# Kernel tuning notes

Hardware: AMD Instinct MI355X
Metric: run time of the kernel (lower is better)

## Reference

```python
import jax, jax.numpy as jnp
import numpy as np

N, E, IN_DIM, H, D = 50000, 1600000, 128, 8, 16


def setup_inputs() -> dict:
    key = jax.random.key(0)
    ks = jax.random.split(key, 9)
    s = 1.0 / np.sqrt(IN_DIM)
    return {
        "h": jax.random.normal(ks[0], (N, IN_DIM), dtype=jnp.float32),
        "Wq": jax.random.normal(ks[1], (IN_DIM, H * D), dtype=jnp.float32) * s,
        "bq": jax.random.normal(ks[2], (H * D,), dtype=jnp.float32) * 0.01,
        "Wk": jax.random.normal(ks[3], (IN_DIM, H * D), dtype=jnp.float32) * s,
        "bk": jax.random.normal(ks[4], (H * D,), dtype=jnp.float32) * 0.01,
        "Wv": jax.random.normal(ks[5], (IN_DIM, H * D), dtype=jnp.float32) * s,
        "bv": jax.random.normal(ks[6], (H * D,), dtype=jnp.float32) * 0.01,
        "src": jax.random.randint(ks[7], (E,), 0, N, dtype=jnp.int32),
        "dst": jax.random.randint(ks[8], (E,), 0, N, dtype=jnp.int32),
    }


def reference(h, Wq, bq, Wk, bk, Wv, bv, src, dst):
    n = h.shape[0]
    # node-level projections, reshaped to [N, H, D]
    Q = (h @ Wq + bq).reshape(n, H, D)
    K = (h @ Wk + bk).reshape(n, H, D)
    V = (h @ Wv + bv).reshape(n, H, D)
    # per-edge score: dot(K[src], Q[dst]) / sqrt(D), exp-clamped -> [E, H]
    score = jnp.sum(K[src] * Q[dst], axis=-1) / np.sqrt(D)
    score = jnp.exp(jnp.clip(score, -5.0, 5.0))
    # score-weighted messages scattered into destination nodes
    m = V[src] * score[:, :, None]                    # [E, H, D]
    wV = jax.ops.segment_sum(m, dst, num_segments=n)  # [N, H, D]
    z = jax.ops.segment_sum(score, dst, num_segments=n)  # [N, H]
    h_out = wV / (z[:, :, None] + 1e-6)
    return h_out.reshape(n, H * D)
```

## Files before the change

### kernel.cpp

```cpp
#include <hip/hip_runtime.h>
#include <hip/hip_bf16.h>

#define IN_DIM 128
#define HH 8
#define DD 16
#define HD 128
#define SCAN_B 256
#define CHUNK 8192

#define MT  64
#define KP  128

typedef float f32x4 __attribute__((ext_vector_type(4)));
typedef short s16x8 __attribute__((ext_vector_type(8)));

__device__ __forceinline__ int sniff_fp32(const unsigned short* h_raw) {
  int sane = 0;
#pragma unroll
  for (int i = 0; i < 128; i += 2) {
    const unsigned short u = h_raw[i];
    const int expo = (u >> 7) & 0xFF;
    if (expo >= 112 && expo <= 143) sane++;
  }
  return (sane >= 40) ? 0 : 1;
}

__global__ __launch_bounds__(128) void wt_kernel(
    const unsigned short* __restrict__ h_raw,
    const void* __restrict__ Wq, const void* __restrict__ Wk,
    const void* __restrict__ Wv, __hip_bfloat16* __restrict__ Wt,
    int* __restrict__ flag, int* __restrict__ bucket_size) {
  const int isf = sniff_fp32(h_raw);
  const int n = blockIdx.x;
  const int k = threadIdx.x;
  if (n == 0) {
    if (k == 0) *flag = isf;
    for (int j = k; j < 258; j += 128) bucket_size[j] = 0;
  }
  const int mat = n >> 7;
  const int col = n & 127;
  const void* W = (mat == 0) ? Wq : (mat == 1) ? Wk : Wv;
  float v;
  if (isf) v = ((const float*)W)[(size_t)k * HD + col];
  else     v = __bfloat162float(((const __hip_bfloat16*)W)[(size_t)k * HD + col]);
  Wt[(size_t)n * KP + k] = __float2bfloat16(v);
}

__global__ __launch_bounds__(256) void proj_hist_kernel(
    const void* __restrict__ h, const __hip_bfloat16* __restrict__ Wt,
    const void* __restrict__ bq, const void* __restrict__ bk,
    const void* __restrict__ bv,
    __hip_bfloat16* __restrict__ Qb, __hip_bfloat16* __restrict__ Kb,
    __hip_bfloat16* __restrict__ Vb,
    const int* __restrict__ flag, int n_nodes,
    const int* __restrict__ dst, int* __restrict__ bucket_size, int n_edges,
    int pgrid) {
  __shared__ int lh[256];

  const int tid = threadIdx.x;

  if (blockIdx.x >= pgrid) {
    const int e0 = (blockIdx.x - pgrid) * CHUNK;
    const int e1 = (e0 + CHUNK < n_edges) ? e0 + CHUNK : n_edges;
    lh[tid] = 0;
    __syncthreads();
    for (int e = e0 + tid; e < e1; e += 256) atomicAdd(&lh[dst[e] >> 8], 1);
    __syncthreads();
    if (lh[tid] > 0) atomicAdd(&bucket_size[tid], lh[tid]);
    return;
  }

  const int node0 = blockIdx.x * MT;
  const int isf = *flag;

  const int wave = tid >> 6;
  const int lane = tid & 63;
  const int l15 = lane & 15;
  const int quad = lane >> 4;

  const int g = node0 + wave * 16 + l15;
  const int gs = (g < n_nodes) ? g : (n_nodes - 1);
  s16x8 afrag[4];
  if (isf) {
    const float* hp = (const float*)h + (size_t)gs * HD;
#pragma unroll
    for (int k4 = 0; k4 < 4; ++k4) {
      const f32x4 a0 = *(const f32x4*)(hp + k4 * 32 + quad * 8);
      const f32x4 a1 = *(const f32x4*)(hp + k4 * 32 + quad * 8 + 4);
      s16x8 fr;
#pragma unroll
      for (int j = 0; j < 4; ++j) {
        const __hip_bfloat16 b0 = __float2bfloat16(a0[j]);
        const __hip_bfloat16 b1 = __float2bfloat16(a1[j]);
        fr[j] = *(const short*)&b0;
        fr[4 + j] = *(const short*)&b1;
      }
      afrag[k4] = fr;
    }
  } else {
    const __hip_bfloat16* hp = (const __hip_bfloat16*)h + (size_t)gs * HD;
#pragma unroll
    for (int k4 = 0; k4 < 4; ++k4)
      afrag[k4] = *(const s16x8*)(hp + k4 * 32 + quad * 8);
  }

  for (int c = 0; c < 3; ++c) {
    const __hip_bfloat16* wb = Wt + (size_t)c * 128 * KP;

    f32x4 acc[8];
#pragma unroll
    for (int t = 0; t < 8; ++t) acc[t] = (f32x4){0.f, 0.f, 0.f, 0.f};

#pragma unroll
    for (int t = 0; t < 8; ++t) {
#pragma unroll
      for (int k4 = 0; k4 < 4; ++k4) {
        const s16x8 bfrag =
            *(const s16x8*)(wb + (t * 16 + l15) * KP + k4 * 32 + quad * 8);
        acc[t] = __builtin_amdgcn_mfma_f32_16x16x32_bf16(afrag[k4], bfrag,
                                                         acc[t], 0, 0, 0);
      }
    }

    const void* bp = (c == 0) ? bq : (c == 1) ? bk : bv;
    __hip_bfloat16* outp = (c == 0) ? Qb : (c == 1) ? Kb : Vb;
#pragma unroll
    for (int t = 0; t < 8; ++t) {
      const int ncol = t * 16 + l15;
      const float bias = isf ? ((const float*)bp)[ncol]
                             : __bfloat162float(((const __hip_bfloat16*)bp)[ncol]);
#pragma unroll
      for (int r = 0; r < 4; ++r) {
        const int gw = node0 + wave * 16 + quad * 4 + r;
        if (gw < n_nodes)
          outp[(size_t)gw * HD + ncol] = __float2bfloat16(acc[t][r] + bias);
      }
    }
  }
}

__global__ __launch_bounds__(256) void bucket_scan_kernel(
    const int* __restrict__ bucket_size, int* __restrict__ bucket_base,
    int* __restrict__ bucket_cur, int nbuck, int n_edges) {
  __shared__ int sh[256];
  const int t = threadIdx.x;
  const int v = (t < nbuck) ? bucket_size[t] : 0;
  sh[t] = v;
  __syncthreads();
  for (int off = 1; off < 256; off <<= 1) {
    int add = (t >= off) ? sh[t - off] : 0;
    __syncthreads();
    sh[t] += add;
    __syncthreads();
  }
  const int excl = sh[t] - v;
  if (t < nbuck) {
    bucket_base[t] = excl;
    bucket_cur[t] = excl;
  }
  if (t == 0) bucket_base[nbuck] = n_edges;
}

__global__ __launch_bounds__(256) void bucketize_kernel(
    const int* __restrict__ src, const int* __restrict__ dst,
    int* __restrict__ bucket_cur, unsigned int* __restrict__ ebuf,
    int n_edges) {
  __shared__ int lh[256];
  const int t = threadIdx.x;
  const int e0 = blockIdx.x * CHUNK;
  const int e1 = (e0 + CHUNK < n_edges) ? e0 + CHUNK : n_edges;
  lh[t] = 0;
  __syncthreads();
  for (int e = e0 + t; e < e1; e += 256) atomicAdd(&lh[dst[e] >> 8], 1);
  __syncthreads();
  const int cnt_local = lh[t];
  int base = 0;
  if (cnt_local > 0) base = atomicAdd(&bucket_cur[t], cnt_local);
  __syncthreads();
  lh[t] = base;
  __syncthreads();
  for (int e = e0 + t; e < e1; e += 256) {
    const int d = dst[e];
    const int pos = atomicAdd(&lh[d >> 8], 1);
    ebuf[pos] = ((unsigned int)src[e] << 16) | (unsigned int)d;
  }
}

__global__ __launch_bounds__(256) void bucket_csr_kernel(
    const unsigned int* __restrict__ ebuf, const int* __restrict__ bucket_base,
    int* __restrict__ row_ptr, int* __restrict__ edge_src,
    int n_nodes, int nbuck) {
  __shared__ int lc[256];
  __shared__ int sh[256];
  const int b = blockIdx.x;
  const int t = threadIdx.x;
  const int lo = bucket_base[b], hi = bucket_base[b + 1];
  const int nbase = b << 8;

  lc[t] = 0;
  __syncthreads();
  for (int i = lo + t; i < hi; i += 256)
    atomicAdd(&lc[(ebuf[i] & 0xFFFFu) - nbase], 1);
  __syncthreads();

  const int v = lc[t];
  sh[t] = v;
  __syncthreads();
  for (int off = 1; off < 256; off <<= 1) {
    int add = (t >= off) ? sh[t - off] : 0;
    __syncthreads();
    sh[t] += add;
    __syncthreads();
  }
  const int excl = sh[t] - v;

  const int node = nbase + t;
  if (node < n_nodes) row_ptr[node] = lo + excl;
  if (b == nbuck - 1 && t == 255) row_ptr[n_nodes] = hi;

  __syncthreads();
  lc[t] = lo + excl;
  __syncthreads();
  for (int i = lo + t; i < hi; i += 256) {
    const unsigned int pkd = ebuf[i];
    const int pos = atomicAdd(&lc[(pkd & 0xFFFFu) - nbase], 1);
    edge_src[pos] = (int)(pkd >> 16);
  }
}

__global__ __launch_bounds__(256) void hist_kernel(
    const int* __restrict__ dst, int* __restrict__ cnt, int n_edges) {
  const int e = blockIdx.x * blockDim.x + threadIdx.x;
  if (e < n_edges) atomicAdd(&cnt[dst[e]], 1);
}

__global__ __launch_bounds__(256) void scatter_kernel(
    const int* __restrict__ src, const int* __restrict__ dst,
    int* __restrict__ cursor, int* __restrict__ edge_src, int n_edges) {
  const int e = blockIdx.x * blockDim.x + threadIdx.x;
  if (e < n_edges) {
    const int pos = atomicAdd(&cursor[dst[e]], 1);
    edge_src[pos] = src[e];
  }
}

__global__ __launch_bounds__(SCAN_B) void scan1_kernel(
    const int* __restrict__ cnt, int* __restrict__ exs,
    int* __restrict__ bsum, int n) {
  __shared__ int sh[SCAN_B];
  const int t = threadIdx.x;
  const int i = blockIdx.x * SCAN_B + t;
  int v = (i < n) ? cnt[i] : 0;
  sh[t] = v;
  __syncthreads();
  for (int off = 1; off < SCAN_B; off <<= 1) {
    int add = (t >= off) ? sh[t - off] : 0;
    __syncthreads();
    sh[t] += add;
    __syncthreads();
  }
  if (i < n) exs[i] = sh[t] - v;
  if (t == SCAN_B - 1) bsum[blockIdx.x] = sh[t];
}

__global__ __launch_bounds__(SCAN_B) void scan2_kernel(int* __restrict__ bsum,
                                                       int nb) {
  __shared__ int sh[SCAN_B];
  const int t = threadIdx.x;
  if (nb <= SCAN_B) {
    int v = (t < nb) ? bsum[t] : 0;
    sh[t] = v;
    __syncthreads();
    for (int off = 1; off < SCAN_B; off <<= 1) {
      int add = (t >= off) ? sh[t - off] : 0;
      __syncthreads();
      sh[t] += add;
      __syncthreads();
    }
    if (t < nb) bsum[t] = sh[t] - v;
  } else if (t == 0) {
    int run = 0;
    for (int b = 0; b < nb; ++b) { int v = bsum[b]; bsum[b] = run; run += v; }
  }
}

__global__ __launch_bounds__(SCAN_B) void scan3_kernel(
    const int* __restrict__ exs, const int* __restrict__ bsum,
    int* __restrict__ row_ptr, int* __restrict__ cursor, int n, int n_edges) {
  const int i = blockIdx.x * SCAN_B + threadIdx.x;
  if (i < n) {
    const int v = exs[i] + bsum[blockIdx.x];
    row_ptr[i] = v;
    cursor[i] = v;
  }
  if (i == 0) row_ptr[n] = n_edges;
}

__global__ __launch_bounds__(128) void gather_kernel(
    const int* __restrict__ row_ptr, const int* __restrict__ edge_src,
    const __hip_bfloat16* __restrict__ Qb, const __hip_bfloat16* __restrict__ Kb,
    const __hip_bfloat16* __restrict__ Vb,
    void* __restrict__ out, const int* __restrict__ flag, int n_nodes) {
  __shared__ float2 sc[2][16 * HH];
  __shared__ float zred[16 * HH];

  const int d = blockIdx.x;
  const int tid = threadIdx.x;

  const int eloc = tid >> 3;
  const int hh8  = tid & 7;
  const int hd16 = tid >> 4;

  const int start = row_ptr[d];
  const int deg = row_ptr[d + 1] - start;

  float qreg[16];
  {
    const uint4* qp = (const uint4*)(Qb + (size_t)d * HD + hh8 * 16);
    unsigned int qw[8];
    *(uint4*)&qw[0] = qp[0];
    *(uint4*)&qw[4] = qp[1];
#pragma unroll
    for (int i = 0; i < 8; ++i) {
      qreg[2 * i]     = __uint_as_float(qw[i] << 16) * 0.25f;
      qreg[2 * i + 1] = __uint_as_float(qw[i] & 0xFFFF0000u) * 0.25f;
    }
  }

  float accV = 0.0f;
  float zacc = 0.0f;
  const int ngroups = (deg + 15) >> 4;

  for (int g = 0; g < ngroups; ++g) {
    const int buf = g & 1;
    const int ei = g * 16 + eloc;

    float score = 0.0f;
    int s = 0;
    if (ei < deg) {
      s = edge_src[start + ei];
      const uint4* kp = (const uint4*)(Kb + (size_t)s * HD + hh8 * 16);
      unsigned int kw[8];
      *(uint4*)&kw[0] = kp[0];
      *(uint4*)&kw[4] = kp[1];
      float dot = 0.0f;
#pragma unroll
      for (int i = 0; i < 8; ++i) {
        const float klo = __uint_as_float(kw[i] << 16);
        const float khi = __uint_as_float(kw[i] & 0xFFFF0000u);
        dot = fmaf(qreg[2 * i], klo, dot);
        dot = fmaf(qreg[2 * i + 1], khi, dot);
      }
      score = __expf(fminf(fmaxf(dot, -5.0f), 5.0f));
    }
    zacc += score;
    sc[buf][eloc * HH + hh8] = make_float2(score, __int_as_float(s));
    __syncthreads();

    const int rem = deg - g * 16;
    const int lim = (rem < 16) ? rem : 16;
    if (lim == 16) {
#pragma unroll
      for (int e = 0; e < 16; ++e) {
        const float2 pe = sc[buf][e * HH + hd16];
        const int s2 = __float_as_int(pe.y);
        const unsigned short vu =
            *(const unsigned short*)(Vb + (size_t)s2 * HD + tid);
        accV = fmaf(pe.x, __uint_as_float(((unsigned int)vu) << 16), accV);
      }
    } else {
      for (int e = 0; e < lim; ++e) {
        const float2 pe = sc[buf][e * HH + hd16];
        const int s2 = __float_as_int(pe.y);
        const unsigned short vu =
            *(const unsigned short*)(Vb + (size_t)s2 * HD + tid);
        accV = fmaf(pe.x, __uint_as_float(((unsigned int)vu) << 16), accV);
      }
    }
  }

  zred[eloc * HH + hh8] = zacc;
  __syncthreads();
  float aZ = 0.0f;
#pragma unroll
  for (int i = 0; i < 16; ++i) aZ += zred[i * HH + hd16];

  const float r = accV / (aZ + 1e-6f);
  const size_t o = (size_t)d * HD + tid;
  if (*flag) ((float*)out)[o] = r;
  else       ((__hip_bfloat16*)out)[o] = __float2bfloat16(r);
}

extern "C" void kernel_launch(void* const* d_in, const int* in_sizes, int n_in,
                              void* d_out, int out_size, void* d_ws, size_t ws_size,
                              hipStream_t stream) {
  const void* h  = d_in[0];
  const void* Wq = d_in[1];
  const void* bq = d_in[2];
  const void* Wk = d_in[3];
  const void* bk = d_in[4];
  const void* Wv = d_in[5];
  const void* bv = d_in[6];
  const int* src = (const int*)d_in[7];
  const int* dst = (const int*)d_in[8];

  const int n_nodes = in_sizes[0] / IN_DIM;
  const int n_edges = in_sizes[7];
  const int nb = (n_nodes + SCAN_B - 1) / SCAN_B;
  const int nbuck = (n_nodes + 255) >> 8;

  char* p = (char*)d_ws;
  int* flag = (int*)p;                       p += 256;
  __hip_bfloat16* Qb = (__hip_bfloat16*)p;   p += (size_t)n_nodes * HD * 2;
  __hip_bfloat16* Kb = (__hip_bfloat16*)p;   p += (size_t)n_nodes * HD * 2;
  __hip_bfloat16* Vb = (__hip_bfloat16*)p;   p += (size_t)n_nodes * HD * 2;
  __hip_bfloat16* Wt = (__hip_bfloat16*)p;   p += ((size_t)384 * KP * 2 + 255) / 256 * 256;
  int* bucket_size = (int*)p;                p += 258 * 4;
  int* bucket_base = (int*)p;                p += 258 * 4;
  int* bucket_cur = (int*)p;                 p += 258 * 4;
  int* row_ptr = (int*)p;                    p += (size_t)(n_nodes + 1) * 4;
  unsigned int* ebuf = (unsigned int*)p;     p += (size_t)n_edges * 4;
  int* edge_src = (int*)p;                   p += (size_t)n_edges * 4;
  int* cnt = (int*)p;                        p += (size_t)n_nodes * 4;
  int* exs = (int*)p;                        p += (size_t)n_nodes * 4;
  int* bsum = (int*)p;                       p += (size_t)(nb + 1) * 4;
  int* cursor = (int*)p;                     p += (size_t)n_nodes * 4;

  wt_kernel<<<384, 128, 0, stream>>>((const unsigned short*)h, Wq, Wk, Wv, Wt,
                                     flag, bucket_size);

  const int pgrid = (n_nodes + MT - 1) / MT;
  const int nchunk = (n_edges + CHUNK - 1) / CHUNK;

  if (n_nodes <= 65536) {
    proj_hist_kernel<<<pgrid + nchunk, 256, 0, stream>>>(
        h, Wt, bq, bk, bv, Qb, Kb, Vb, flag, n_nodes, dst, bucket_size,
        n_edges, pgrid);
    bucket_scan_kernel<<<1, 256, 0, stream>>>(bucket_size, bucket_base,
                                              bucket_cur, nbuck, n_edges);
    bucketize_kernel<<<nchunk, 256, 0, stream>>>(src, dst, bucket_cur, ebuf,
                                                 n_edges);
    bucket_csr_kernel<<<nbuck, 256, 0, stream>>>(ebuf, bucket_base, row_ptr,
                                                 edge_src, n_nodes, nbuck);
  } else {
    proj_hist_kernel<<<pgrid, 256, 0, stream>>>(
        h, Wt, bq, bk, bv, Qb, Kb, Vb, flag, n_nodes, dst, bucket_size,
        n_edges, pgrid);
    hipMemsetAsync(cnt, 0, (size_t)n_nodes * sizeof(int), stream);
    const int eb = 256;
    const int egrid = (n_edges + eb - 1) / eb;
    hist_kernel<<<egrid, eb, 0, stream>>>(dst, cnt, n_edges);
    scan1_kernel<<<nb, SCAN_B, 0, stream>>>(cnt, exs, bsum, n_nodes);
    scan2_kernel<<<1, SCAN_B, 0, stream>>>(bsum, nb);
    scan3_kernel<<<nb, SCAN_B, 0, stream>>>(exs, bsum, row_ptr, cursor,
                                            n_nodes, n_edges);
    scatter_kernel<<<egrid, eb, 0, stream>>>(src, dst, cursor, edge_src,
                                             n_edges);
  }

  gather_kernel<<<n_nodes, 128, 0, stream>>>(row_ptr, edge_src, Qb, Kb, Vb,
                                             d_out, flag, n_nodes);
}
```

Before: 325.1 us.

## Fuse bucket scan into histogram, register-cache bucketize, pack two nodes per gather block

The bucket prefix scan is folded into the histogram blocks of the projection kernel: the last chunk to finish, detected with an atomic counter, performs the scan, which removes one kernel launch. Bucketize now uses smaller chunks and keeps the packed src/dst words in registers, so the second pass no longer rereads src and dst from global memory. The gather kernel processes two destination nodes per 256-thread block and prefetches the next edge_src index a group ahead. Both halves of a block loop to the larger of the two degrees, so some work is wasted on imbalanced node pairs, and the last-block scan depends on correct fence and atomic ordering.

```diff
diff --git a/kernel.cpp b/kernel.cpp
--- a/kernel.cpp
+++ b/kernel.cpp
@@ -7,6 +7,7 @@
 #define HD 128
 #define SCAN_B 256
 #define CHUNK 8192
+#define CHUNK2 2048
 
 #define MT  64
 #define KP  128
@@ -53,24 +54,50 @@
     __hip_bfloat16* __restrict__ Qb, __hip_bfloat16* __restrict__ Kb,
     __hip_bfloat16* __restrict__ Vb,
     const int* __restrict__ flag, int n_nodes,
-    const int* __restrict__ dst, int* __restrict__ bucket_size, int n_edges,
-    int pgrid) {
+    const int* __restrict__ dst, int* __restrict__ bucket_size,
+    int* __restrict__ bucket_base, int* __restrict__ bucket_cur,
+    int n_edges, int nchunk, int nbuck) {
   __shared__ int lh[256];
+  __shared__ int sh[256];
+  __shared__ int is_last;
 
   const int tid = threadIdx.x;
 
-  if (blockIdx.x >= pgrid) {
-    const int e0 = (blockIdx.x - pgrid) * CHUNK;
+  if (blockIdx.x < nchunk) {
+    const int e0 = blockIdx.x * CHUNK;
     const int e1 = (e0 + CHUNK < n_edges) ? e0 + CHUNK : n_edges;
     lh[tid] = 0;
     __syncthreads();
     for (int e = e0 + tid; e < e1; e += 256) atomicAdd(&lh[dst[e] >> 8], 1);
     __syncthreads();
     if (lh[tid] > 0) atomicAdd(&bucket_size[tid], lh[tid]);
+    __threadfence();
+    if (tid == 0) {
+      const int old = atomicAdd(&bucket_size[256], 1);
+      is_last = (old == nchunk - 1);
+    }
+    __syncthreads();
+    if (!is_last) return;
+
+    const int v = (tid < nbuck) ? atomicAdd(&bucket_size[tid], 0) : 0;
+    sh[tid] = v;
+    __syncthreads();
+    for (int off = 1; off < 256; off <<= 1) {
+      int add = (tid >= off) ? sh[tid - off] : 0;
+      __syncthreads();
+      sh[tid] += add;
+      __syncthreads();
+    }
+    const int excl = sh[tid] - v;
+    if (tid < nbuck) {
+      bucket_base[tid] = excl;
+      bucket_cur[tid] = excl;
+    }
+    if (tid == 0) bucket_base[nbuck] = n_edges;
     return;
   }
 
-  const int node0 = blockIdx.x * MT;
+  const int node0 = (blockIdx.x - nchunk) * MT;
   const int isf = *flag;
 
   const int wave = tid >> 6;
@@ -137,28 +164,6 @@
       }
     }
   }
-}
-
-__global__ __launch_bounds__(256) void bucket_scan_kernel(
-    const int* __restrict__ bucket_size, int* __restrict__ bucket_base,
-    int* __restrict__ bucket_cur, int nbuck, int n_edges) {
-  __shared__ int sh[256];
-  const int t = threadIdx.x;
-  const int v = (t < nbuck) ? bucket_size[t] : 0;
-  sh[t] = v;
-  __syncthreads();
-  for (int off = 1; off < 256; off <<= 1) {
-    int add = (t >= off) ? sh[t - off] : 0;
-    __syncthreads();
-    sh[t] += add;
-    __syncthreads();
-  }
-  const int excl = sh[t] - v;
-  if (t < nbuck) {
-    bucket_base[t] = excl;
-    bucket_cur[t] = excl;
-  }
-  if (t == 0) bucket_base[nbuck] = n_edges;
 }
 
 __global__ __launch_bounds__(256) void bucketize_kernel(
@@ -167,11 +172,20 @@
     int n_edges) {
   __shared__ int lh[256];
   const int t = threadIdx.x;
-  const int e0 = blockIdx.x * CHUNK;
-  const int e1 = (e0 + CHUNK < n_edges) ? e0 + CHUNK : n_edges;
+  const int e0 = blockIdx.x * CHUNK2;
+  const int e1 = (e0 + CHUNK2 < n_edges) ? e0 + CHUNK2 : n_edges;
   lh[t] = 0;
   __syncthreads();
-  for (int e = e0 + t; e < e1; e += 256) atomicAdd(&lh[dst[e] >> 8], 1);
+  unsigned int pk[CHUNK2 / 256];
+#pragma unroll
+  for (int j = 0; j < CHUNK2 / 256; ++j) {
+    const int e = e0 + j * 256 + t;
+    if (e < e1) {
+      const int d = dst[e];
+      pk[j] = ((unsigned int)src[e] << 16) | (unsigned int)d;
+      atomicAdd(&lh[d >> 8], 1);
+    }
+  }
   __syncthreads();
   const int cnt_local = lh[t];
   int base = 0;
@@ -179,10 +193,13 @@
   __syncthreads();
   lh[t] = base;
   __syncthreads();
-  for (int e = e0 + t; e < e1; e += 256) {
-    const int d = dst[e];
-    const int pos = atomicAdd(&lh[d >> 8], 1);
-    ebuf[pos] = ((unsigned int)src[e] << 16) | (unsigned int)d;
+#pragma unroll
+  for (int j = 0; j < CHUNK2 / 256; ++j) {
+    const int e = e0 + j * 256 + t;
+    if (e < e1) {
+      const int pos = atomicAdd(&lh[(pk[j] & 0xFFFFu) >> 8], 1);
+      ebuf[pos] = pk[j];
+    }
   }
 }
 
@@ -296,27 +313,35 @@
   if (i == 0) row_ptr[n] = n_edges;
 }
 
-__global__ __launch_bounds__(128) void gather_kernel(
+__global__ __launch_bounds__(256, 8) void gather_kernel(
     const int* __restrict__ row_ptr, const int* __restrict__ edge_src,
     const __hip_bfloat16* __restrict__ Qb, const __hip_bfloat16* __restrict__ Kb,
     const __hip_bfloat16* __restrict__ Vb,
     void* __restrict__ out, const int* __restrict__ flag, int n_nodes) {
-  __shared__ float2 sc[2][16 * HH];
-  __shared__ float zred[16 * HH];
-
-  const int d = blockIdx.x;
+  __shared__ float2 sc[2][2][16 * HH];
+  __shared__ float zred[2][16 * HH];
+  __shared__ int dsh[2];
+
   const int tid = threadIdx.x;
-
-  const int eloc = tid >> 3;
-  const int hh8  = tid & 7;
-  const int hd16 = tid >> 4;
-
-  const int start = row_ptr[d];
-  const int deg = row_ptr[d + 1] - start;
+  const int half = tid >> 7;
+  const int t1 = tid & 127;
+
+  const int eloc = t1 >> 3;
+  const int hh8  = t1 & 7;
+  const int hd16 = t1 >> 4;
+
+  const int d = 2 * blockIdx.x + half;
+  const int valid = (d < n_nodes);
+  const int dc = valid ? d : (n_nodes - 1);
+
+  const int start = row_ptr[dc];
+  const int deg = valid ? (row_ptr[dc + 1] - start) : 0;
+
+  if (t1 == 0) dsh[half] = deg;
 
   float qreg[16];
   {
-    const uint4* qp = (const uint4*)(Qb + (size_t)d * HD + hh8 * 16);
+    const uint4* qp = (const uint4*)(Qb + (size_t)dc * HD + hh8 * 16);
     unsigned int qw[8];
     *(uint4*)&qw[0] = qp[0];
     *(uint4*)&qw[4] = qp[1];
@@ -327,18 +352,24 @@
     }
   }
 
+  __syncthreads();
+  const int ngm = ((dsh[0] > dsh[1] ? dsh[0] : dsh[1]) + 15) >> 4;
+
   float accV = 0.0f;
   float zacc = 0.0f;
-  const int ngroups = (deg + 15) >> 4;
-
-  for (int g = 0; g < ngroups; ++g) {
+
+  int s_cur = (eloc < deg) ? edge_src[start + eloc] : 0;
+
+  for (int g = 0; g < ngm; ++g) {
     const int buf = g & 1;
     const int ei = g * 16 + eloc;
 
+    const int ei_n = ei + 16;
+    const int s_nxt = (ei_n < deg) ? edge_src[start + ei_n] : 0;
+
     float score = 0.0f;
-    int s = 0;
+    const int s = s_cur;
     if (ei < deg) {
-      s = edge_src[start + ei];
       const uint4* kp = (const uint4*)(Kb + (size_t)s * HD + hh8 * 16);
       unsigned int kw[8];
       *(uint4*)&kw[0] = kp[0];
@@ -354,7 +385,7 @@
       score = __expf(fminf(fmaxf(dot, -5.0f), 5.0f));
     }
     zacc += score;
-    sc[buf][eloc * HH + hh8] = make_float2(score, __int_as_float(s));
+    sc[half][buf][eloc * HH + hh8] = make_float2(score, __int_as_float(s));
     __syncthreads();
 
     const int rem = deg - g * 16;
@@ -362,33 +393,36 @@
     if (lim == 16) {
 #pragma unroll
       for (int e = 0; e < 16; ++e) {
-        const float2 pe = sc[buf][e * HH + hd16];
+        const float2 pe = sc[half][buf][e * HH + hd16];
         const int s2 = __float_as_int(pe.y);
         const unsigned short vu =
-            *(const unsigned short*)(Vb + (size_t)s2 * HD + tid);
+            *(const unsigned short*)(Vb + (size_t)s2 * HD + t1);
         accV = fmaf(pe.x, __uint_as_float(((unsigned int)vu) << 16), accV);
       }
     } else {
       for (int e = 0; e < lim; ++e) {
-        const float2 pe = sc[buf][e * HH + hd16];
+        const float2 pe = sc[half][buf][e * HH + hd16];
         const int s2 = __float_as_int(pe.y);
         const unsigned short vu =
-            *(const unsigned short*)(Vb + (size_t)s2 * HD + tid);
+            *(const unsigned short*)(Vb + (size_t)s2 * HD + t1);
         accV = fmaf(pe.x, __uint_as_float(((unsigned int)vu) << 16), accV);
       }
     }
-  }
-
-  zred[eloc * HH + hh8] = zacc;
+    s_cur = s_nxt;
+  }
+
+  zred[half][eloc * HH + hh8] = zacc;
   __syncthreads();
   float aZ = 0.0f;
 #pragma unroll
-  for (int i = 0; i < 16; ++i) aZ += zred[i * HH + hd16];
-
-  const float r = accV / (aZ + 1e-6f);
-  const size_t o = (size_t)d * HD + tid;
-  if (*flag) ((float*)out)[o] = r;
-  else       ((__hip_bfloat16*)out)[o] = __float2bfloat16(r);
+  for (int i = 0; i < 16; ++i) aZ += zred[half][i * HH + hd16];
+
+  if (valid) {
+    const float r = accV / (aZ + 1e-6f);
+    const size_t o = (size_t)d * HD + t1;
+    if (*flag) ((float*)out)[o] = r;
+    else       ((__hip_bfloat16*)out)[o] = __float2bfloat16(r);
+  }
 }
 
 extern "C" void kernel_launch(void* const* d_in, const int* in_sizes, int n_in,
@@ -433,19 +467,18 @@
   const int nchunk = (n_edges + CHUNK - 1) / CHUNK;
 
   if (n_nodes <= 65536) {
-    proj_hist_kernel<<<pgrid + nchunk, 256, 0, stream>>>(
+    proj_hist_kernel<<<nchunk + pgrid, 256, 0, stream>>>(
         h, Wt, bq, bk, bv, Qb, Kb, Vb, flag, n_nodes, dst, bucket_size,
-        n_edges, pgrid);
-    bucket_scan_kernel<<<1, 256, 0, stream>>>(bucket_size, bucket_base,
-                                              bucket_cur, nbuck, n_edges);
-    bucketize_kernel<<<nchunk, 256, 0, stream>>>(src, dst, bucket_cur, ebuf,
-                                                 n_edges);
+        bucket_base, bucket_cur, n_edges, nchunk, nbuck);
+    const int nchunk2 = (n_edges + CHUNK2 - 1) / CHUNK2;
+    bucketize_kernel<<<nchunk2, 256, 0, stream>>>(src, dst, bucket_cur, ebuf,
+                                                  n_edges);
     bucket_csr_kernel<<<nbuck, 256, 0, stream>>>(ebuf, bucket_base, row_ptr,
                                                  edge_src, n_nodes, nbuck);
   } else {
     proj_hist_kernel<<<pgrid, 256, 0, stream>>>(
         h, Wt, bq, bk, bv, Qb, Kb, Vb, flag, n_nodes, dst, bucket_size,
-        n_edges, pgrid);
+        bucket_base, bucket_cur, n_edges, 0, nbuck);
     hipMemsetAsync(cnt, 0, (size_t)n_nodes * sizeof(int), stream);
     const int eb = 256;
     const int egrid = (n_edges + eb - 1) / eb;
@@ -458,6 +491,7 @@
                                              n_edges);
   }
 
-  gather_kernel<<<n_nodes, 128, 0, stream>>>(row_ptr, edge_src, Qb, Kb, Vb,
-                                             d_out, flag, n_nodes);
-}
+  const int ggrid = (n_nodes + 1) / 2;
+  gather_kernel<<<ggrid, 256, 0, stream>>>(row_ptr, edge_src, Qb, Kb, Vb,
+                                           d_out, flag, n_nodes);
+}
```

Measured after the change: 417.9 us. +28.5%, slower.
